# Kernel optimization log

Hardware: AMD Instinct MI355X
Metric: run time of the kernel (lower is better)

Reference implementation:

```python
import jax, jax.numpy as jnp
import numpy as np


def _fake_quant(x, bits, axis):
    """AQT-style abs-max symmetric fake quantization.

    IntNumerics(bits, preserve_zero=True, preserve_max_val=True, clip=True,
    round=True) with AbsMaxCalibration: bound = 2^(bits-1)-1,
    scale = absmax/bound (stop-gradient), q = round(clip(x/scale)),
    dequant = q*scale. Round uses straight-through estimator.
    """
    bound = float(2 ** (bits - 1) - 1)
    absmax = jax.lax.stop_gradient(
        jnp.max(jnp.abs(x), axis=axis, keepdims=True))
    scale = absmax / bound
    scale = jnp.where(scale == 0.0, jnp.ones_like(scale), scale)
    s = x / scale
    clipped = jnp.clip(s, -bound, bound)  # clip_gradient=True semantics
    rounded = clipped + jax.lax.stop_gradient(jnp.round(clipped) - clipped)
    return rounded * scale


def setup_inputs() -> dict:
    key = jax.random.key(0)
    k1, k2, k3 = jax.random.split(key, 3)
    B, S, D, F = 4, 2048, 4096, 4096
    x = jax.random.normal(k1, (B, S, D), dtype=jnp.float32)
    # lecun_normal over (in, out)
    kernel = jax.random.normal(k2, (D, F), dtype=jnp.float32) / np.sqrt(D)
    bias = jax.random.normal(k3, (F,), dtype=jnp.float32) * 0.01
    return {"x": x, "kernel": kernel, "bias": bias}


def reference(x, kernel, bias):
    # int8 fake-quant of activations: abs-max over contracting (last) axis
    xq = _fake_quant(x, bits=8, axis=-1)
    # int8 fake-quant of kernel: abs-max over contracting axis (0) -> per out-col
    kq = _fake_quant(kernel, bits=8, axis=0)
    # quantized dot_general: contract last axis of x with axis 0 of kernel
    y = jnp.einsum('bsd,df->bsf', xq, kq)
    # int16 fake-quant of bias (calibration_axes=-1 over the whole vector)
    bq16 = _fake_quant(bias, bits=16, axis=-1)
    y = y + bq16[None, None, :]
    # int8 output requant, per-row abs-max over feature axis
    out = _fake_quant(y, bits=8, axis=-1)
    return out
```

## Files before the change

### kernel.cpp

```cpp
#include <hip/hip_runtime.h>
#include <stdint.h>

typedef int int32x4 __attribute__((ext_vector_type(4)));

#define M_ROWS 8192
#define K_DIM  4096
#define N_DIM  4096

#define GPTR(p) ((const __attribute__((address_space(1))) unsigned int*)(p))
#define LPTR(p) ((__attribute__((address_space(3))) unsigned int*)(p))

__device__ __forceinline__ float block_absmax_256(float v, float* red) {
#pragma unroll
  for (int off = 32; off > 0; off >>= 1)
    v = fmaxf(v, __shfl_down(v, off, 64));
  const int w = threadIdx.x >> 6;
  if ((threadIdx.x & 63) == 0) red[w] = v;
  __syncthreads();
  return fmaxf(fmaxf(red[0], red[1]), fmaxf(red[2], red[3]));
}

__global__ void quant_x_kernel(const float* __restrict__ x,
                               int8_t* __restrict__ qx,
                               float* __restrict__ sx) {
  __shared__ float red[4];
  const int row = blockIdx.x;
  const int t = threadIdx.x;
  const float* xr = x + (size_t)row * K_DIM;
  float4 v[4];
  float m = 0.0f;
#pragma unroll
  for (int i = 0; i < 4; ++i) {
    v[i] = *(const float4*)(xr + t * 16 + i * 4);
    m = fmaxf(m, fmaxf(fmaxf(fabsf(v[i].x), fabsf(v[i].y)),
                       fmaxf(fabsf(v[i].z), fabsf(v[i].w))));
  }
  float amax = block_absmax_256(m, red);
  float scale = amax / 127.0f;
  if (scale == 0.0f) scale = 1.0f;
  if (t == 0) sx[row] = scale;
  int words[4];
#pragma unroll
  for (int i = 0; i < 4; ++i) {
    float a = fminf(fmaxf(v[i].x / scale, -127.0f), 127.0f);
    float b = fminf(fmaxf(v[i].y / scale, -127.0f), 127.0f);
    float c = fminf(fmaxf(v[i].z / scale, -127.0f), 127.0f);
    float d = fminf(fmaxf(v[i].w / scale, -127.0f), 127.0f);
    int qa = (int)rintf(a), qb = (int)rintf(b), qc = (int)rintf(c), qd = (int)rintf(d);
    words[i] = (qa & 255) | ((qb & 255) << 8) | ((qc & 255) << 16) | ((qd & 255) << 24);
  }
  *(int4*)(qx + (size_t)row * K_DIM + t * 16) =
      make_int4(words[0], words[1], words[2], words[3]);
}

__global__ void colmax_kernel(const float* __restrict__ k,
                              unsigned int* __restrict__ cm) {
  const int c = blockIdx.x * 256 + threadIdx.x;
  const int r0 = blockIdx.y * 128;
  float m = 0.0f;
  for (int i = 0; i < 128; ++i)
    m = fmaxf(m, fabsf(k[(size_t)(r0 + i) * N_DIM + c]));
  atomicMax(&cm[c], __float_as_uint(m));
}

__global__ void finalize_kernel(const float* __restrict__ cm,
                                float* __restrict__ sk,
                                const float* __restrict__ bias,
                                float* __restrict__ bq) {
  __shared__ float red[4];
  const int t = threadIdx.x;
  if (blockIdx.x < 16) {
    const int c = blockIdx.x * 256 + t;
    float s = cm[c] / 127.0f;
    if (s == 0.0f) s = 1.0f;
    sk[c] = s;
  } else {
    float4 v[4];
    float m = 0.0f;
#pragma unroll
    for (int i = 0; i < 4; ++i) {
      v[i] = *(const float4*)(bias + t * 16 + i * 4);
      m = fmaxf(m, fmaxf(fmaxf(fabsf(v[i].x), fabsf(v[i].y)),
                         fmaxf(fabsf(v[i].z), fabsf(v[i].w))));
    }
    float amax = block_absmax_256(m, red);
    float s = amax / 32767.0f;
    if (s == 0.0f) s = 1.0f;
#pragma unroll
    for (int i = 0; i < 4; ++i) {
      float4 o;
      o.x = rintf(fminf(fmaxf(v[i].x / s, -32767.0f), 32767.0f)) * s;
      o.y = rintf(fminf(fmaxf(v[i].y / s, -32767.0f), 32767.0f)) * s;
      o.z = rintf(fminf(fmaxf(v[i].z / s, -32767.0f), 32767.0f)) * s;
      o.w = rintf(fminf(fmaxf(v[i].w / s, -32767.0f), 32767.0f)) * s;
      *(float4*)(bq + t * 16 + i * 4) = o;
    }
  }
}

__global__ void quant_kT_kernel(const float* __restrict__ kern,
                                const float* __restrict__ cm,
                                int8_t* __restrict__ qkT) {
  __shared__ int8_t tile[64][80];
  const int t = threadIdx.x;
  const int c0 = blockIdx.x * 64;
  const int r0 = blockIdx.y * 64;
  const int colg = (t & 15) * 4;
  const int row = t >> 4;
  float s[4];
#pragma unroll
  for (int j = 0; j < 4; ++j) {
    float v = cm[c0 + colg + j] / 127.0f;
    s[j] = (v == 0.0f) ? 1.0f : v;
  }
#pragma unroll
  for (int i = 0; i < 4; ++i) {
    const int r = row + i * 16;
    float4 v = *(const float4*)&kern[(size_t)(r0 + r) * N_DIM + c0 + colg];
    tile[colg + 0][r] = (int8_t)rintf(fminf(fmaxf(v.x / s[0], -127.0f), 127.0f));
    tile[colg + 1][r] = (int8_t)rintf(fminf(fmaxf(v.y / s[1], -127.0f), 127.0f));
    tile[colg + 2][r] = (int8_t)rintf(fminf(fmaxf(v.z / s[2], -127.0f), 127.0f));
    tile[colg + 3][r] = (int8_t)rintf(fminf(fmaxf(v.w / s[3], -127.0f), 127.0f));
  }
  __syncthreads();
  const int f = t >> 2;
  const int seg = (t & 3) * 16;
  int4 w = *(const int4*)&tile[f][seg];
  *(int4*)(qkT + (size_t)(c0 + f) * K_DIM + r0 + seg) = w;
}

#define BM 128
#define BN 128
#define BK 128

__global__ void gemm_kernel(const int8_t* __restrict__ qx,
                            const int8_t* __restrict__ qkT,
                            const float* __restrict__ sx,
                            const float* __restrict__ sk,
                            const float* __restrict__ bq,
                            float* __restrict__ out) {
  __shared__ int32x4 AsV[1024];
  __shared__ int32x4 BsV[1024];
  char* As = (char*)AsV;
  char* Bs = (char*)BsV;

  const int t = threadIdx.x;
  const int w = t >> 6;
  const int l = t & 63;
  const int wm = w >> 1, wn = w & 1;
  const int rowBase = blockIdx.y * BM;
  const int colBase = blockIdx.x * BN;

  const int8_t* gA = qx  + (size_t)(rowBase + (l >> 3)) * K_DIM
                         + (((l & 7) ^ (l >> 3)) * 16);
  const int8_t* gB = qkT + (size_t)(colBase + (l >> 3)) * K_DIM
                         + (((l & 7) ^ (l >> 3)) * 16);

  int arow[4], brow[4], soff[2];
#pragma unroll
  for (int mt = 0; mt < 4; ++mt)
    arow[mt] = (wm * 64 + mt * 16 + (l & 15)) * 128;
#pragma unroll
  for (int nt = 0; nt < 4; ++nt)
    brow[nt] = (wn * 64 + nt * 16 + (l & 15)) * 128;
#pragma unroll
  for (int s = 0; s < 2; ++s)
    soff[s] = ((s * 4 + (l >> 4)) ^ (l & 7)) * 16;

  int32x4 zero = {0, 0, 0, 0};
  int32x4 acc[4][4];
#pragma unroll
  for (int mt = 0; mt < 4; ++mt)
#pragma unroll
    for (int nt = 0; nt < 4; ++nt) acc[mt][nt] = zero;

  for (int k0 = 0; k0 < K_DIM; k0 += BK) {
    __syncthreads();
#pragma unroll
    for (int j = 0; j < 4; ++j) {
      const int ca = j * 4 + w;
      __builtin_amdgcn_global_load_lds(
          GPTR(gA + (size_t)ca * 8 * K_DIM + k0),
          LPTR(As + ca * 1024), 16, 0, 0);
      __builtin_amdgcn_global_load_lds(
          GPTR(gB + (size_t)ca * 8 * K_DIM + k0),
          LPTR(Bs + ca * 1024), 16, 0, 0);
    }
    __syncthreads();

#pragma unroll
    for (int s = 0; s < 2; ++s) {
      int32x4 af[4], bf[4];
#pragma unroll
      for (int mt = 0; mt < 4; ++mt)
        af[mt] = *(const int32x4*)(As + arow[mt] + soff[s]);
#pragma unroll
      for (int nt = 0; nt < 4; ++nt)
        bf[nt] = *(const int32x4*)(Bs + brow[nt] + soff[s]);
#pragma unroll
      for (int mt = 0; mt < 4; ++mt)
#pragma unroll
        for (int nt = 0; nt < 4; ++nt)
          acc[mt][nt] = __builtin_amdgcn_mfma_i32_16x16x64_i8(
              af[mt], bf[nt], acc[mt][nt], 0, 0, 0);
    }
  }

  const int lr = (l >> 4) * 4;
  const int lc = l & 15;
#pragma unroll
  for (int mt = 0; mt < 4; ++mt) {
    const int r0 = rowBase + wm * 64 + mt * 16 + lr;
    float sxr[4];
#pragma unroll
    for (int r = 0; r < 4; ++r) sxr[r] = sx[r0 + r];
#pragma unroll
    for (int nt = 0; nt < 4; ++nt) {
      const int c = colBase + wn * 64 + nt * 16 + lc;
      const float skc = sk[c];
      const float bqc = bq[c];
#pragma unroll
      for (int r = 0; r < 4; ++r)
        out[(size_t)(r0 + r) * N_DIM + c] =
            (float)acc[mt][nt][r] * (sxr[r] * skc) + bqc;
    }
  }
}

__global__ void requant_kernel(float* __restrict__ y) {
  __shared__ float red[4];
  const int row = blockIdx.x;
  const int t = threadIdx.x;
  float* yr = y + (size_t)row * N_DIM;
  float4 v[4];
  float m = 0.0f;
#pragma unroll
  for (int i = 0; i < 4; ++i) {
    v[i] = *(const float4*)(yr + i * 1024 + t * 4);
    m = fmaxf(m, fmaxf(fmaxf(fabsf(v[i].x), fabsf(v[i].y)),
                       fmaxf(fabsf(v[i].z), fabsf(v[i].w))));
  }
  float amax = block_absmax_256(m, red);
  float s = amax / 127.0f;
  if (s == 0.0f) s = 1.0f;
#pragma unroll
  for (int i = 0; i < 4; ++i) {
    float4 o;
    o.x = rintf(fminf(fmaxf(v[i].x / s, -127.0f), 127.0f)) * s;
    o.y = rintf(fminf(fmaxf(v[i].y / s, -127.0f), 127.0f)) * s;
    o.z = rintf(fminf(fmaxf(v[i].z / s, -127.0f), 127.0f)) * s;
    o.w = rintf(fminf(fmaxf(v[i].w / s, -127.0f), 127.0f)) * s;
    *(float4*)(yr + i * 1024 + t * 4) = o;
  }
}

extern "C" void kernel_launch(void* const* d_in, const int* in_sizes, int n_in,
                              void* d_out, int out_size, void* d_ws, size_t ws_size,
                              hipStream_t stream) {
  (void)in_sizes; (void)n_in; (void)out_size; (void)ws_size;
  const float* x    = (const float*)d_in[0];
  const float* kern = (const float*)d_in[1];
  const float* bias = (const float*)d_in[2];
  float* out = (float*)d_out;

  char* w8 = (char*)d_ws;
  int8_t* qx  = (int8_t*)w8;
  int8_t* qkT = (int8_t*)(w8 + 33554432);
  float* sx   = (float*)(w8 + 50331648);
  float* cm   = (float*)(w8 + 50331648 + 32768);
  float* sk   = (float*)(w8 + 50331648 + 49152);
  float* bq   = (float*)(w8 + 50331648 + 65536);

  hipMemsetAsync(cm, 0, 4096 * sizeof(float), stream);
  quant_x_kernel<<<M_ROWS, 256, 0, stream>>>(x, qx, sx);
  colmax_kernel<<<dim3(16, 32), 256, 0, stream>>>(kern, (unsigned int*)cm);
  finalize_kernel<<<17, 256, 0, stream>>>(cm, sk, bias, bq);
  quant_kT_kernel<<<dim3(64, 64), 256, 0, stream>>>(kern, cm, qkT);
  gemm_kernel<<<dim3(N_DIM / BN, M_ROWS / BM), 256, 0, stream>>>(qx, qkT, sx, sk, bq, out);
  requant_kernel<<<M_ROWS, 256, 0, stream>>>(out);
}
```

Baseline: 469.3 us.

## Use 32x32x32 int8 MFMA, XCD-aware tile mapping, and deterministic column max

The GEMM switches from 16x16x64 to 32x32x32 int8 MFMA with 2x2 accumulator tiles per wave, which cuts LDS fragment reads per MFMA. Block IDs are remapped so each XCD works on a contiguous group of column tiles to improve L2 reuse of B. The atomicMax column-max pass and its memset are replaced by per-chunk partial maxima reduced in the finalize kernel. The quant kernels use coalesced strided float4 loads instead of 16-element-per-thread chunks, and quant_kT now reads the precomputed scales.

```diff
diff --git a/kernel.cpp b/kernel.cpp
--- a/kernel.cpp
+++ b/kernel.cpp
@@ -1,7 +1,8 @@
 #include <hip/hip_runtime.h>
 #include <stdint.h>
 
-typedef int int32x4 __attribute__((ext_vector_type(4)));
+typedef int int32x4  __attribute__((ext_vector_type(4)));
+typedef int int32x16 __attribute__((ext_vector_type(16)));
 
 #define M_ROWS 8192
 #define K_DIM  4096
@@ -31,7 +32,7 @@
   float m = 0.0f;
 #pragma unroll
   for (int i = 0; i < 4; ++i) {
-    v[i] = *(const float4*)(xr + t * 16 + i * 4);
+    v[i] = *(const float4*)(xr + i * 1024 + t * 4);
     m = fmaxf(m, fmaxf(fmaxf(fabsf(v[i].x), fabsf(v[i].y)),
                        fmaxf(fabsf(v[i].z), fabsf(v[i].w))));
   }
@@ -39,7 +40,6 @@
   float scale = amax / 127.0f;
   if (scale == 0.0f) scale = 1.0f;
   if (t == 0) sx[row] = scale;
-  int words[4];
 #pragma unroll
   for (int i = 0; i < 4; ++i) {
     float a = fminf(fmaxf(v[i].x / scale, -127.0f), 127.0f);
@@ -47,23 +47,22 @@
     float c = fminf(fmaxf(v[i].z / scale, -127.0f), 127.0f);
     float d = fminf(fmaxf(v[i].w / scale, -127.0f), 127.0f);
     int qa = (int)rintf(a), qb = (int)rintf(b), qc = (int)rintf(c), qd = (int)rintf(d);
-    words[i] = (qa & 255) | ((qb & 255) << 8) | ((qc & 255) << 16) | ((qd & 255) << 24);
-  }
-  *(int4*)(qx + (size_t)row * K_DIM + t * 16) =
-      make_int4(words[0], words[1], words[2], words[3]);
+    int word = (qa & 255) | ((qb & 255) << 8) | ((qc & 255) << 16) | ((qd & 255) << 24);
+    *(int*)(qx + (size_t)row * K_DIM + i * 1024 + t * 4) = word;
+  }
 }
 
 __global__ void colmax_kernel(const float* __restrict__ k,
-                              unsigned int* __restrict__ cm) {
+                              float* __restrict__ pm) {
   const int c = blockIdx.x * 256 + threadIdx.x;
   const int r0 = blockIdx.y * 128;
   float m = 0.0f;
   for (int i = 0; i < 128; ++i)
     m = fmaxf(m, fabsf(k[(size_t)(r0 + i) * N_DIM + c]));
-  atomicMax(&cm[c], __float_as_uint(m));
-}
-
-__global__ void finalize_kernel(const float* __restrict__ cm,
+  pm[(size_t)blockIdx.y * N_DIM + c] = m;
+}
+
+__global__ void finalize_kernel(const float* __restrict__ pm,
                                 float* __restrict__ sk,
                                 const float* __restrict__ bias,
                                 float* __restrict__ bq) {
@@ -71,7 +70,10 @@
   const int t = threadIdx.x;
   if (blockIdx.x < 16) {
     const int c = blockIdx.x * 256 + t;
-    float s = cm[c] / 127.0f;
+    float m = 0.0f;
+#pragma unroll
+    for (int i = 0; i < 32; ++i) m = fmaxf(m, pm[(size_t)i * N_DIM + c]);
+    float s = m / 127.0f;
     if (s == 0.0f) s = 1.0f;
     sk[c] = s;
   } else {
@@ -79,7 +81,7 @@
     float m = 0.0f;
 #pragma unroll
     for (int i = 0; i < 4; ++i) {
-      v[i] = *(const float4*)(bias + t * 16 + i * 4);
+      v[i] = *(const float4*)(bias + i * 1024 + t * 4);
       m = fmaxf(m, fmaxf(fmaxf(fabsf(v[i].x), fabsf(v[i].y)),
                          fmaxf(fabsf(v[i].z), fabsf(v[i].w))));
     }
@@ -93,13 +95,13 @@
       o.y = rintf(fminf(fmaxf(v[i].y / s, -32767.0f), 32767.0f)) * s;
       o.z = rintf(fminf(fmaxf(v[i].z / s, -32767.0f), 32767.0f)) * s;
       o.w = rintf(fminf(fmaxf(v[i].w / s, -32767.0f), 32767.0f)) * s;
-      *(float4*)(bq + t * 16 + i * 4) = o;
+      *(float4*)(bq + i * 1024 + t * 4) = o;
     }
   }
 }
 
 __global__ void quant_kT_kernel(const float* __restrict__ kern,
-                                const float* __restrict__ cm,
+                                const float* __restrict__ sk,
                                 int8_t* __restrict__ qkT) {
   __shared__ int8_t tile[64][80];
   const int t = threadIdx.x;
@@ -109,10 +111,7 @@
   const int row = t >> 4;
   float s[4];
 #pragma unroll
-  for (int j = 0; j < 4; ++j) {
-    float v = cm[c0 + colg + j] / 127.0f;
-    s[j] = (v == 0.0f) ? 1.0f : v;
-  }
+  for (int j = 0; j < 4; ++j) s[j] = sk[c0 + colg + j];
 #pragma unroll
   for (int i = 0; i < 4; ++i) {
     const int r = row + i * 16;
@@ -148,31 +147,36 @@
   const int w = t >> 6;
   const int l = t & 63;
   const int wm = w >> 1, wn = w & 1;
-  const int rowBase = blockIdx.y * BM;
-  const int colBase = blockIdx.x * BN;
+
+  const int id = blockIdx.x;
+  const int xcd = id & 7;
+  const int seq = id >> 3;
+  const int rowBase = (seq & 63) * BM;
+  const int colBase = (xcd * 4 + (seq >> 6)) * BN;
 
   const int8_t* gA = qx  + (size_t)(rowBase + (l >> 3)) * K_DIM
                          + (((l & 7) ^ (l >> 3)) * 16);
   const int8_t* gB = qkT + (size_t)(colBase + (l >> 3)) * K_DIM
                          + (((l & 7) ^ (l >> 3)) * 16);
 
-  int arow[4], brow[4], soff[2];
-#pragma unroll
-  for (int mt = 0; mt < 4; ++mt)
-    arow[mt] = (wm * 64 + mt * 16 + (l & 15)) * 128;
-#pragma unroll
-  for (int nt = 0; nt < 4; ++nt)
-    brow[nt] = (wn * 64 + nt * 16 + (l & 15)) * 128;
-#pragma unroll
-  for (int s = 0; s < 2; ++s)
-    soff[s] = ((s * 4 + (l >> 4)) ^ (l & 7)) * 16;
-
-  int32x4 zero = {0, 0, 0, 0};
-  int32x4 acc[4][4];
-#pragma unroll
-  for (int mt = 0; mt < 4; ++mt)
-#pragma unroll
-    for (int nt = 0; nt < 4; ++nt) acc[mt][nt] = zero;
+  int arow[2], brow[2], soff[4];
+#pragma unroll
+  for (int mt = 0; mt < 2; ++mt)
+    arow[mt] = (wm * 64 + mt * 32 + (l & 31)) * 128;
+#pragma unroll
+  for (int nt = 0; nt < 2; ++nt)
+    brow[nt] = (wn * 64 + nt * 32 + (l & 31)) * 128;
+#pragma unroll
+  for (int s = 0; s < 4; ++s)
+    soff[s] = ((s * 2 + (l >> 5)) ^ (l & 7)) * 16;
+
+  int32x16 acc[2][2];
+#pragma unroll
+  for (int mt = 0; mt < 2; ++mt)
+#pragma unroll
+    for (int nt = 0; nt < 2; ++nt)
+#pragma unroll
+      for (int r = 0; r < 16; ++r) acc[mt][nt][r] = 0;
 
   for (int k0 = 0; k0 < K_DIM; k0 += BK) {
     __syncthreads();
@@ -189,40 +193,43 @@
     __syncthreads();
 
 #pragma unroll
-    for (int s = 0; s < 2; ++s) {
-      int32x4 af[4], bf[4];
-#pragma unroll
-      for (int mt = 0; mt < 4; ++mt)
+    for (int s = 0; s < 4; ++s) {
+      int32x4 af[2], bf[2];
+#pragma unroll
+      for (int mt = 0; mt < 2; ++mt)
         af[mt] = *(const int32x4*)(As + arow[mt] + soff[s]);
 #pragma unroll
-      for (int nt = 0; nt < 4; ++nt)
+      for (int nt = 0; nt < 2; ++nt)
         bf[nt] = *(const int32x4*)(Bs + brow[nt] + soff[s]);
 #pragma unroll
-      for (int mt = 0; mt < 4; ++mt)
-#pragma unroll
-        for (int nt = 0; nt < 4; ++nt)
-          acc[mt][nt] = __builtin_amdgcn_mfma_i32_16x16x64_i8(
+      for (int mt = 0; mt < 2; ++mt)
+#pragma unroll
+        for (int nt = 0; nt < 2; ++nt)
+          acc[mt][nt] = __builtin_amdgcn_mfma_i32_32x32x32_i8(
               af[mt], bf[nt], acc[mt][nt], 0, 0, 0);
     }
   }
 
-  const int lr = (l >> 4) * 4;
-  const int lc = l & 15;
-#pragma unroll
-  for (int mt = 0; mt < 4; ++mt) {
-    const int r0 = rowBase + wm * 64 + mt * 16 + lr;
-    float sxr[4];
-#pragma unroll
-    for (int r = 0; r < 4; ++r) sxr[r] = sx[r0 + r];
-#pragma unroll
-    for (int nt = 0; nt < 4; ++nt) {
-      const int c = colBase + wn * 64 + nt * 16 + lc;
+  const int l5 = (l >> 5) * 4;
+  const int lc = l & 31;
+#pragma unroll
+  for (int mt = 0; mt < 2; ++mt) {
+    const int rbase = rowBase + wm * 64 + mt * 32;
+    float sxr[16];
+#pragma unroll
+    for (int reg = 0; reg < 16; ++reg)
+      sxr[reg] = sx[rbase + (reg & 3) + 8 * (reg >> 2) + l5];
+#pragma unroll
+    for (int nt = 0; nt < 2; ++nt) {
+      const int c = colBase + wn * 64 + nt * 32 + lc;
       const float skc = sk[c];
       const float bqc = bq[c];
 #pragma unroll
-      for (int r = 0; r < 4; ++r)
-        out[(size_t)(r0 + r) * N_DIM + c] =
-            (float)acc[mt][nt][r] * (sxr[r] * skc) + bqc;
+      for (int reg = 0; reg < 16; ++reg) {
+        const int r = rbase + (reg & 3) + 8 * (reg >> 2) + l5;
+        out[(size_t)r * N_DIM + c] =
+            (float)acc[mt][nt][reg] * (sxr[reg] * skc) + bqc;
+      }
     }
   }
 }
@@ -267,15 +274,14 @@
   int8_t* qx  = (int8_t*)w8;
   int8_t* qkT = (int8_t*)(w8 + 33554432);
   float* sx   = (float*)(w8 + 50331648);
-  float* cm   = (float*)(w8 + 50331648 + 32768);
   float* sk   = (float*)(w8 + 50331648 + 49152);
   float* bq   = (float*)(w8 + 50331648 + 65536);
-
-  hipMemsetAsync(cm, 0, 4096 * sizeof(float), stream);
+  float* pm   = (float*)(w8 + 50331648 + 131072);
+
   quant_x_kernel<<<M_ROWS, 256, 0, stream>>>(x, qx, sx);
-  colmax_kernel<<<dim3(16, 32), 256, 0, stream>>>(kern, (unsigned int*)cm);
-  finalize_kernel<<<17, 256, 0, stream>>>(cm, sk, bias, bq);
-  quant_kT_kernel<<<dim3(64, 64), 256, 0, stream>>>(kern, cm, qkT);
-  gemm_kernel<<<dim3(N_DIM / BN, M_ROWS / BM), 256, 0, stream>>>(qx, qkT, sx, sk, bq, out);
+  colmax_kernel<<<dim3(16, 32), 256, 0, stream>>>(kern, pm);
+  finalize_kernel<<<17, 256, 0, stream>>>(pm, sk, bias, bq);
+  quant_kT_kernel<<<dim3(64, 64), 256, 0, stream>>>(kern, sk, qkT);
+  gemm_kernel<<<2048, 256, 0, stream>>>(qx, qkT, sx, sk, bq, out);
   requant_kernel<<<M_ROWS, 256, 0, stream>>>(out);
 }
```

Result: slower. 510.4 us (+8.8%).

## Merge prep kernels, drop atomics, and double-buffer GEMM LDS loads

Applied to the files above, without the earlier changes.

Merges activation quantization, kernel column-max partials and bias quantization into one launch. Per-block column maxima are written to a partial buffer and reduced inside the transpose-quantize kernel, which removes the memset and the atomics. The GEMM main loop now double-buffers LDS, prefetching the next K tile while the current one is consumed, and drops one barrier per iteration. This doubles GEMM shared memory, which may lower occupancy, and the x loads are restructured into coalesced strided float4 reads.

```diff
diff --git a/kernel.cpp b/kernel.cpp
--- a/kernel.cpp
+++ b/kernel.cpp
@@ -20,66 +20,55 @@
   return fmaxf(fmaxf(red[0], red[1]), fmaxf(red[2], red[3]));
 }
 
-__global__ void quant_x_kernel(const float* __restrict__ x,
-                               int8_t* __restrict__ qx,
-                               float* __restrict__ sx) {
+__global__ void prep_kernel(const float* __restrict__ x,
+                            const float* __restrict__ kern,
+                            const float* __restrict__ bias,
+                            int8_t* __restrict__ qx,
+                            float* __restrict__ sx,
+                            float* __restrict__ pm,
+                            float* __restrict__ bq) {
   __shared__ float red[4];
-  const int row = blockIdx.x;
-  const int t = threadIdx.x;
-  const float* xr = x + (size_t)row * K_DIM;
-  float4 v[4];
-  float m = 0.0f;
-#pragma unroll
-  for (int i = 0; i < 4; ++i) {
-    v[i] = *(const float4*)(xr + t * 16 + i * 4);
-    m = fmaxf(m, fmaxf(fmaxf(fabsf(v[i].x), fabsf(v[i].y)),
-                       fmaxf(fabsf(v[i].z), fabsf(v[i].w))));
-  }
-  float amax = block_absmax_256(m, red);
-  float scale = amax / 127.0f;
-  if (scale == 0.0f) scale = 1.0f;
-  if (t == 0) sx[row] = scale;
-  int words[4];
-#pragma unroll
-  for (int i = 0; i < 4; ++i) {
-    float a = fminf(fmaxf(v[i].x / scale, -127.0f), 127.0f);
-    float b = fminf(fmaxf(v[i].y / scale, -127.0f), 127.0f);
-    float c = fminf(fmaxf(v[i].z / scale, -127.0f), 127.0f);
-    float d = fminf(fmaxf(v[i].w / scale, -127.0f), 127.0f);
-    int qa = (int)rintf(a), qb = (int)rintf(b), qc = (int)rintf(c), qd = (int)rintf(d);
-    words[i] = (qa & 255) | ((qb & 255) << 8) | ((qc & 255) << 16) | ((qd & 255) << 24);
-  }
-  *(int4*)(qx + (size_t)row * K_DIM + t * 16) =
-      make_int4(words[0], words[1], words[2], words[3]);
-}
-
-__global__ void colmax_kernel(const float* __restrict__ k,
-                              unsigned int* __restrict__ cm) {
-  const int c = blockIdx.x * 256 + threadIdx.x;
-  const int r0 = blockIdx.y * 128;
-  float m = 0.0f;
-  for (int i = 0; i < 128; ++i)
-    m = fmaxf(m, fabsf(k[(size_t)(r0 + i) * N_DIM + c]));
-  atomicMax(&cm[c], __float_as_uint(m));
-}
-
-__global__ void finalize_kernel(const float* __restrict__ cm,
-                                float* __restrict__ sk,
-                                const float* __restrict__ bias,
-                                float* __restrict__ bq) {
-  __shared__ float red[4];
-  const int t = threadIdx.x;
-  if (blockIdx.x < 16) {
-    const int c = blockIdx.x * 256 + t;
-    float s = cm[c] / 127.0f;
-    if (s == 0.0f) s = 1.0f;
-    sk[c] = s;
+  const int t = threadIdx.x;
+  const int b = blockIdx.x;
+
+  if (b < M_ROWS) {
+    const float* xr = x + (size_t)b * K_DIM;
+    float4 v[4];
+    float m = 0.0f;
+#pragma unroll
+    for (int i = 0; i < 4; ++i) {
+      v[i] = *(const float4*)(xr + i * 1024 + t * 4);
+      m = fmaxf(m, fmaxf(fmaxf(fabsf(v[i].x), fabsf(v[i].y)),
+                         fmaxf(fabsf(v[i].z), fabsf(v[i].w))));
+    }
+    float amax = block_absmax_256(m, red);
+    float scale = amax / 127.0f;
+    if (scale == 0.0f) scale = 1.0f;
+    if (t == 0) sx[b] = scale;
+#pragma unroll
+    for (int i = 0; i < 4; ++i) {
+      float a = fminf(fmaxf(v[i].x / scale, -127.0f), 127.0f);
+      float bb = fminf(fmaxf(v[i].y / scale, -127.0f), 127.0f);
+      float c = fminf(fmaxf(v[i].z / scale, -127.0f), 127.0f);
+      float d = fminf(fmaxf(v[i].w / scale, -127.0f), 127.0f);
+      int qa = (int)rintf(a), qb = (int)rintf(bb), qc = (int)rintf(c), qd = (int)rintf(d);
+      int word = (qa & 255) | ((qb & 255) << 8) | ((qc & 255) << 16) | ((qd & 255) << 24);
+      *(int*)(qx + (size_t)b * K_DIM + i * 1024 + t * 4) = word;
+    }
+  } else if (b < M_ROWS + 512) {
+    const int bb = b - M_ROWS;
+    const int c = (bb & 15) * 256 + t;
+    const int r0 = (bb >> 4) * 128;
+    float m = 0.0f;
+    for (int i = 0; i < 128; ++i)
+      m = fmaxf(m, fabsf(kern[(size_t)(r0 + i) * N_DIM + c]));
+    pm[(size_t)(bb >> 4) * N_DIM + c] = m;
   } else {
     float4 v[4];
     float m = 0.0f;
 #pragma unroll
     for (int i = 0; i < 4; ++i) {
-      v[i] = *(const float4*)(bias + t * 16 + i * 4);
+      v[i] = *(const float4*)(bias + i * 1024 + t * 4);
       m = fmaxf(m, fmaxf(fmaxf(fabsf(v[i].x), fabsf(v[i].y)),
                          fmaxf(fabsf(v[i].z), fabsf(v[i].w))));
     }
@@ -93,26 +82,35 @@
       o.y = rintf(fminf(fmaxf(v[i].y / s, -32767.0f), 32767.0f)) * s;
       o.z = rintf(fminf(fmaxf(v[i].z / s, -32767.0f), 32767.0f)) * s;
       o.w = rintf(fminf(fmaxf(v[i].w / s, -32767.0f), 32767.0f)) * s;
-      *(float4*)(bq + t * 16 + i * 4) = o;
+      *(float4*)(bq + i * 1024 + t * 4) = o;
     }
   }
 }
 
 __global__ void quant_kT_kernel(const float* __restrict__ kern,
-                                const float* __restrict__ cm,
+                                const float* __restrict__ pm,
+                                float* __restrict__ sk,
                                 int8_t* __restrict__ qkT) {
   __shared__ int8_t tile[64][80];
+  __shared__ float skl[64];
   const int t = threadIdx.x;
   const int c0 = blockIdx.x * 64;
   const int r0 = blockIdx.y * 64;
+  if (t < 64) {
+    float m = 0.0f;
+#pragma unroll
+    for (int i = 0; i < 32; ++i) m = fmaxf(m, pm[(size_t)i * N_DIM + c0 + t]);
+    float s = m / 127.0f;
+    if (s == 0.0f) s = 1.0f;
+    skl[t] = s;
+    if (blockIdx.y == 0) sk[c0 + t] = s;
+  }
+  __syncthreads();
   const int colg = (t & 15) * 4;
   const int row = t >> 4;
   float s[4];
 #pragma unroll
-  for (int j = 0; j < 4; ++j) {
-    float v = cm[c0 + colg + j] / 127.0f;
-    s[j] = (v == 0.0f) ? 1.0f : v;
-  }
+  for (int j = 0; j < 4; ++j) s[j] = skl[colg + j];
 #pragma unroll
   for (int i = 0; i < 4; ++i) {
     const int r = row + i * 16;
@@ -139,8 +137,8 @@
                             const float* __restrict__ sk,
                             const float* __restrict__ bq,
                             float* __restrict__ out) {
-  __shared__ int32x4 AsV[1024];
-  __shared__ int32x4 BsV[1024];
+  __shared__ int32x4 AsV[2048];
+  __shared__ int32x4 BsV[2048];
   char* As = (char*)AsV;
   char* Bs = (char*)BsV;
 
@@ -174,29 +172,44 @@
 #pragma unroll
     for (int nt = 0; nt < 4; ++nt) acc[mt][nt] = zero;
 
+#pragma unroll
+  for (int j = 0; j < 4; ++j) {
+    const int ca = j * 4 + w;
+    __builtin_amdgcn_global_load_lds(GPTR(gA + (size_t)ca * 8 * K_DIM),
+                                     LPTR(As + ca * 1024), 16, 0, 0);
+    __builtin_amdgcn_global_load_lds(GPTR(gB + (size_t)ca * 8 * K_DIM),
+                                     LPTR(Bs + ca * 1024), 16, 0, 0);
+  }
+
+#pragma unroll 2
   for (int k0 = 0; k0 < K_DIM; k0 += BK) {
+    const int p = (k0 >> 7) & 1;
+    const int pb = p * 16384;
     __syncthreads();
-#pragma unroll
-    for (int j = 0; j < 4; ++j) {
-      const int ca = j * 4 + w;
-      __builtin_amdgcn_global_load_lds(
-          GPTR(gA + (size_t)ca * 8 * K_DIM + k0),
-          LPTR(As + ca * 1024), 16, 0, 0);
-      __builtin_amdgcn_global_load_lds(
-          GPTR(gB + (size_t)ca * 8 * K_DIM + k0),
-          LPTR(Bs + ca * 1024), 16, 0, 0);
-    }
-    __syncthreads();
+
+    if (k0 + BK < K_DIM) {
+      const int qb = (p ^ 1) * 16384;
+#pragma unroll
+      for (int j = 0; j < 4; ++j) {
+        const int ca = j * 4 + w;
+        __builtin_amdgcn_global_load_lds(
+            GPTR(gA + (size_t)ca * 8 * K_DIM + k0 + BK),
+            LPTR(As + qb + ca * 1024), 16, 0, 0);
+        __builtin_amdgcn_global_load_lds(
+            GPTR(gB + (size_t)ca * 8 * K_DIM + k0 + BK),
+            LPTR(Bs + qb + ca * 1024), 16, 0, 0);
+      }
+    }
 
 #pragma unroll
     for (int s = 0; s < 2; ++s) {
       int32x4 af[4], bf[4];
 #pragma unroll
       for (int mt = 0; mt < 4; ++mt)
-        af[mt] = *(const int32x4*)(As + arow[mt] + soff[s]);
+        af[mt] = *(const int32x4*)(As + pb + arow[mt] + soff[s]);
 #pragma unroll
       for (int nt = 0; nt < 4; ++nt)
-        bf[nt] = *(const int32x4*)(Bs + brow[nt] + soff[s]);
+        bf[nt] = *(const int32x4*)(Bs + pb + brow[nt] + soff[s]);
 #pragma unroll
       for (int mt = 0; mt < 4; ++mt)
 #pragma unroll
@@ -267,15 +280,12 @@
   int8_t* qx  = (int8_t*)w8;
   int8_t* qkT = (int8_t*)(w8 + 33554432);
   float* sx   = (float*)(w8 + 50331648);
-  float* cm   = (float*)(w8 + 50331648 + 32768);
   float* sk   = (float*)(w8 + 50331648 + 49152);
   float* bq   = (float*)(w8 + 50331648 + 65536);
-
-  hipMemsetAsync(cm, 0, 4096 * sizeof(float), stream);
-  quant_x_kernel<<<M_ROWS, 256, 0, stream>>>(x, qx, sx);
-  colmax_kernel<<<dim3(16, 32), 256, 0, stream>>>(kern, (unsigned int*)cm);
-  finalize_kernel<<<17, 256, 0, stream>>>(cm, sk, bias, bq);
-  quant_kT_kernel<<<dim3(64, 64), 256, 0, stream>>>(kern, cm, qkT);
+  float* pm   = (float*)(w8 + 50331648 + 131072);
+
+  prep_kernel<<<M_ROWS + 512 + 1, 256, 0, stream>>>(x, kern, bias, qx, sx, pm, bq);
+  quant_kT_kernel<<<dim3(64, 64), 256, 0, stream>>>(kern, pm, sk, qkT);
   gemm_kernel<<<dim3(N_DIM / BN, M_ROWS / BM), 256, 0, stream>>>(qx, qkT, sx, sk, bq, out);
   requant_kernel<<<M_ROWS, 256, 0, stream>>>(out);
 }
```

Result: slower. 478.8 us (+2.0%).
